# Optimization experiments

Measured on AMD Instinct MI355X. Metric: run time of the kernel, lower is better.

## Reference

```python
import jax, jax.numpy as jnp
import numpy as np

B = 2097152  # number of Gaussians


def setup_inputs() -> dict:
    key = jax.random.key(0)
    k1, k2, k3, k4, k5, k6 = jax.random.split(key, 6)
    return {
        "loc1": jax.random.normal(k1, (B, 3), dtype=jnp.float32),
        "scale1": jax.random.uniform(k2, (B, 3), dtype=jnp.float32),
        "rot_matrix1": jax.random.normal(k3, (B, 3, 3), dtype=jnp.float32),
        "loc2": jax.random.normal(k4, (B, 3), dtype=jnp.float32),
        "scale2": jax.random.uniform(k5, (B, 3), dtype=jnp.float32),
        "rot_matrix2": jax.random.normal(k6, (B, 3, 3), dtype=jnp.float32),
    }


def reference(loc1, scale1, rot_matrix1, loc2, scale2, rot_matrix2):
    # ||mu1 - mu2||^2  -> (B,)
    loc_diff2 = jnp.sum((loc1 - loc2) ** 2, axis=-1)

    # cov2 = R2 diag(scale2) R2^T  -> (B,3,3)
    cov2 = jnp.einsum("bij,bj,bkj->bik", rot_matrix2, scale2, rot_matrix2)
    # cov2 rotated into frame of Gaussian 1: R1^T cov2 R1  -> (B,3,3)
    cov2_R1 = jnp.einsum("bji,bjk,bkl->bil", rot_matrix1, cov2, rot_matrix1)

    # E = diag(sqrt(s1)) cov2_R1 diag(sqrt(s1)), then symmetrize
    s1_sqrt = jnp.sqrt(scale1)  # (B,3)
    E = s1_sqrt[:, :, None] * cov2_R1 * s1_sqrt[:, None, :]
    E = (E + jnp.swapaxes(E, 1, 2)) * 0.5

    # trace of matrix sqrt via eigenvalues: sum (lambda^2)^(1/4) = sum |lambda|^(1/2)
    E_eig = jnp.linalg.eigvalsh(E)  # (B,3)
    E_sqrt_trace = jnp.sum(jnp.sqrt(jnp.sqrt(E_eig ** 2)), axis=-1)

    cov_wasserstein = jnp.sum(scale1, axis=-1) + jnp.sum(scale2, axis=-1) - 2.0 * E_sqrt_trace
    cov_wasserstein = jnp.maximum(cov_wasserstein, 0.0)
    return jnp.sqrt(loc_diff2 + cov_wasserstein)
```

## Files before the change

kernel.cpp:

```cpp
#include <hip/hip_runtime.h>
#include <math.h>

#define BLK 256

__global__ __launch_bounds__(BLK, 8) void wasserstein_kernel(
    const float* __restrict__ loc1,   const float* __restrict__ scale1,
    const float* __restrict__ rot1,   const float* __restrict__ loc2,
    const float* __restrict__ scale2, const float* __restrict__ rot2,
    float* __restrict__ out)
{
    __shared__ float smem[BLK * 18];
    float* sR1 = smem;
    float* sR2 = smem + BLK * 9;

    const int tid = threadIdx.x;
    const long long blockStart = (long long)blockIdx.x * BLK;
    const long long idx = blockStart + tid;

    {
        const float4* g4;
        float4* l4;

        g4 = reinterpret_cast<const float4*>(rot1 + blockStart * 9);
        l4 = reinterpret_cast<float4*>(sR1);
#pragma unroll
        for (int i = 0; i < BLK * 9 / 4 / BLK + 1; ++i) {
            int j = tid + i * BLK;
            if (j < BLK * 9 / 4) l4[j] = g4[j];
        }

        g4 = reinterpret_cast<const float4*>(rot2 + blockStart * 9);
        l4 = reinterpret_cast<float4*>(sR2);
#pragma unroll
        for (int i = 0; i < BLK * 9 / 4 / BLK + 1; ++i) {
            int j = tid + i * BLK;
            if (j < BLK * 9 / 4) l4[j] = g4[j];
        }
    }

    const float l1x = loc1[idx * 3 + 0], l1y = loc1[idx * 3 + 1], l1z = loc1[idx * 3 + 2];
    const float l2x = loc2[idx * 3 + 0], l2y = loc2[idx * 3 + 1], l2z = loc2[idx * 3 + 2];
    const float s1a = scale1[idx * 3 + 0], s1b = scale1[idx * 3 + 1], s1c = scale1[idx * 3 + 2];
    const float s2a = scale2[idx * 3 + 0], s2b = scale2[idx * 3 + 1], s2c = scale2[idx * 3 + 2];

    __syncthreads();

    const float dx = l1x - l2x, dy = l1y - l2y, dz = l1z - l2z;
    const float loc_diff2 = dx * dx + dy * dy + dz * dz;

    float R1[9], R2[9];
#pragma unroll
    for (int k = 0; k < 9; ++k) R1[k] = sR1[tid * 9 + k];
#pragma unroll
    for (int k = 0; k < 9; ++k) R2[k] = sR2[tid * 9 + k];

    const float m00 = s2a * R2[0] * R2[0] + s2b * R2[1] * R2[1] + s2c * R2[2] * R2[2];
    const float m01 = s2a * R2[0] * R2[3] + s2b * R2[1] * R2[4] + s2c * R2[2] * R2[5];
    const float m02 = s2a * R2[0] * R2[6] + s2b * R2[1] * R2[7] + s2c * R2[2] * R2[8];
    const float m11 = s2a * R2[3] * R2[3] + s2b * R2[4] * R2[4] + s2c * R2[5] * R2[5];
    const float m12 = s2a * R2[3] * R2[6] + s2b * R2[4] * R2[7] + s2c * R2[5] * R2[8];
    const float m22 = s2a * R2[6] * R2[6] + s2b * R2[7] * R2[7] + s2c * R2[8] * R2[8];

    float A[9];
    A[0] = m00 * R1[0] + m01 * R1[3] + m02 * R1[6];
    A[1] = m00 * R1[1] + m01 * R1[4] + m02 * R1[7];
    A[2] = m00 * R1[2] + m01 * R1[5] + m02 * R1[8];
    A[3] = m01 * R1[0] + m11 * R1[3] + m12 * R1[6];
    A[4] = m01 * R1[1] + m11 * R1[4] + m12 * R1[7];
    A[5] = m01 * R1[2] + m11 * R1[5] + m12 * R1[8];
    A[6] = m02 * R1[0] + m12 * R1[3] + m22 * R1[6];
    A[7] = m02 * R1[1] + m12 * R1[4] + m22 * R1[7];
    A[8] = m02 * R1[2] + m12 * R1[5] + m22 * R1[8];

    float T[9];
    T[0] = R1[0] * A[0] + R1[3] * A[3] + R1[6] * A[6];
    T[1] = R1[0] * A[1] + R1[3] * A[4] + R1[6] * A[7];
    T[2] = R1[0] * A[2] + R1[3] * A[5] + R1[6] * A[8];
    T[3] = R1[1] * A[0] + R1[4] * A[3] + R1[7] * A[6];
    T[4] = R1[1] * A[1] + R1[4] * A[4] + R1[7] * A[7];
    T[5] = R1[1] * A[2] + R1[4] * A[5] + R1[7] * A[8];
    T[6] = R1[2] * A[0] + R1[5] * A[3] + R1[8] * A[6];
    T[7] = R1[2] * A[1] + R1[5] * A[4] + R1[8] * A[7];
    T[8] = R1[2] * A[2] + R1[5] * A[5] + R1[8] * A[8];

    const float sq0 = sqrtf(s1a), sq1 = sqrtf(s1b), sq2 = sqrtf(s1c);
    const float e00 = s1a * T[0];
    const float e11 = s1b * T[4];
    const float e22 = s1c * T[8];
    const float e01 = 0.5f * sq0 * sq1 * (T[1] + T[3]);
    const float e02 = 0.5f * sq0 * sq2 * (T[2] + T[6]);
    const float e12 = 0.5f * sq1 * sq2 * (T[5] + T[7]);

    const float q  = (e00 + e11 + e22) * (1.0f / 3.0f);
    const float p1 = e01 * e01 + e02 * e02 + e12 * e12;
    const float d0 = e00 - q, d1 = e11 - q, d2 = e22 - q;
    const float p2 = d0 * d0 + d1 * d1 + d2 * d2 + 2.0f * p1;

    float trace_sqrt;
    if (p2 > 1e-24f) {
        const float p   = sqrtf(p2 * (1.0f / 6.0f));
        const float inv = 1.0f / p;
        const float b00 = d0 * inv, b11 = d1 * inv, b22 = d2 * inv;
        const float b01 = e01 * inv, b02 = e02 * inv, b12 = e12 * inv;
        float detB = b00 * (b11 * b22 - b12 * b12)
                   - b01 * (b01 * b22 - b12 * b02)
                   + b02 * (b01 * b12 - b11 * b02);
        float r = 0.5f * detB;
        r = fminf(fmaxf(r, -1.0f), 1.0f);
        const float phi  = acosf(r) * (1.0f / 3.0f);
        const float twop = 2.0f * p;
        const float eig1 = q + twop * cosf(phi);
        const float eig3 = q + twop * cosf(phi + 2.0943951023931953f);
        const float eig2 = 3.0f * q - eig1 - eig3;
        trace_sqrt = sqrtf(fabsf(eig1)) + sqrtf(fabsf(eig2)) + sqrtf(fabsf(eig3));
    } else {
        trace_sqrt = 3.0f * sqrtf(fabsf(q));
    }

    float cov_w = (s1a + s1b + s1c) + (s2a + s2b + s2c) - 2.0f * trace_sqrt;
    cov_w = fmaxf(cov_w, 0.0f);
    out[idx] = sqrtf(loc_diff2 + cov_w);
}

extern "C" void kernel_launch(void* const* d_in, const int* in_sizes, int n_in,
                              void* d_out, int out_size, void* d_ws, size_t ws_size,
                              hipStream_t stream) {
    const float* loc1   = (const float*)d_in[0];
    const float* scale1 = (const float*)d_in[1];
    const float* rot1   = (const float*)d_in[2];
    const float* loc2   = (const float*)d_in[3];
    const float* scale2 = (const float*)d_in[4];
    const float* rot2   = (const float*)d_in[5];
    float* out = (float*)d_out;

    const int B = in_sizes[0] / 3;
    const int grid = B / BLK;

    wasserstein_kernel<<<grid, BLK, 0, stream>>>(loc1, scale1, rot1,
                                                 loc2, scale2, rot2, out);
}
```

Baseline: 240.2 us.

## Process four elements per thread with software-pipelined loads and characteristic-polynomial eigen solve

Result: no change. 241.6 us (+0.6%).

```diff
diff --git a/kernel.cpp b/kernel.cpp
--- a/kernel.cpp
+++ b/kernel.cpp
@@ -3,123 +3,121 @@
 
 #define BLK 256
 
-__global__ __launch_bounds__(BLK, 8) void wasserstein_kernel(
+struct Elem {
+    float l1[3], l2[3], s1[3], s2[3], R1[9], R2[9];
+};
+
+__device__ __forceinline__ void load_elem(
+    const float* __restrict__ loc1, const float* __restrict__ scale1,
+    const float* __restrict__ rot1, const float* __restrict__ loc2,
+    const float* __restrict__ scale2, const float* __restrict__ rot2,
+    int idx, Elem& e)
+{
+    __builtin_memcpy(e.R1, rot1   + (size_t)idx * 9, 36);
+    __builtin_memcpy(e.R2, rot2   + (size_t)idx * 9, 36);
+    __builtin_memcpy(e.l1, loc1   + (size_t)idx * 3, 12);
+    __builtin_memcpy(e.l2, loc2   + (size_t)idx * 3, 12);
+    __builtin_memcpy(e.s1, scale1 + (size_t)idx * 3, 12);
+    __builtin_memcpy(e.s2, scale2 + (size_t)idx * 3, 12);
+}
+
+__device__ __forceinline__ float compute(const Elem& e)
+{
+    const float dx = e.l1[0] - e.l2[0];
+    const float dy = e.l1[1] - e.l2[1];
+    const float dz = e.l1[2] - e.l2[2];
+    const float ld2 = dx * dx + dy * dy + dz * dz;
+
+    const float* R1 = e.R1;
+    const float* R2 = e.R2;
+    const float sa = e.s1[0], sb = e.s1[1], sc = e.s1[2];
+    const float ua = e.s2[0], ub = e.s2[1], uc = e.s2[2];
+
+    const float m00 = ua * R2[0] * R2[0] + ub * R2[1] * R2[1] + uc * R2[2] * R2[2];
+    const float m01 = ua * R2[0] * R2[3] + ub * R2[1] * R2[4] + uc * R2[2] * R2[5];
+    const float m02 = ua * R2[0] * R2[6] + ub * R2[1] * R2[7] + uc * R2[2] * R2[8];
+    const float m11 = ua * R2[3] * R2[3] + ub * R2[4] * R2[4] + uc * R2[5] * R2[5];
+    const float m12 = ua * R2[3] * R2[6] + ub * R2[4] * R2[7] + uc * R2[5] * R2[8];
+    const float m22 = ua * R2[6] * R2[6] + ub * R2[7] * R2[7] + uc * R2[8] * R2[8];
+
+    const float A0 = m00 * R1[0] + m01 * R1[3] + m02 * R1[6];
+    const float A1 = m00 * R1[1] + m01 * R1[4] + m02 * R1[7];
+    const float A2 = m00 * R1[2] + m01 * R1[5] + m02 * R1[8];
+    const float A3 = m01 * R1[0] + m11 * R1[3] + m12 * R1[6];
+    const float A4 = m01 * R1[1] + m11 * R1[4] + m12 * R1[7];
+    const float A5 = m01 * R1[2] + m11 * R1[5] + m12 * R1[8];
+    const float A6 = m02 * R1[0] + m12 * R1[3] + m22 * R1[6];
+    const float A7 = m02 * R1[1] + m12 * R1[4] + m22 * R1[7];
+    const float A8 = m02 * R1[2] + m12 * R1[5] + m22 * R1[8];
+
+    const float t00 = R1[0] * A0 + R1[3] * A3 + R1[6] * A6;
+    const float t01 = R1[0] * A1 + R1[3] * A4 + R1[6] * A7;
+    const float t02 = R1[0] * A2 + R1[3] * A5 + R1[6] * A8;
+    const float t11 = R1[1] * A1 + R1[4] * A4 + R1[7] * A7;
+    const float t12 = R1[1] * A2 + R1[4] * A5 + R1[7] * A8;
+    const float t22 = R1[2] * A2 + R1[5] * A5 + R1[8] * A8;
+
+    const float c2 = t00 * sa + t11 * sb + t22 * sc;
+    const float g2 = t00 * t00 * sa * sa + t11 * t11 * sb * sb + t22 * t22 * sc * sc
+                   + 2.0f * (t01 * t01 * sa * sb + t02 * t02 * sa * sc + t12 * t12 * sb * sc);
+    const float c1 = 0.5f * (c2 * c2 - g2);
+    const float detT = t00 * (t11 * t22 - t12 * t12)
+                     - t01 * (t01 * t22 - t12 * t02)
+                     + t02 * (t01 * t12 - t11 * t02);
+    const float c0 = detT * sa * sb * sc;
+
+    const float m  = c2 * (1.0f / 3.0f);
+    const float p  = c1 - c2 * m;
+    const float q  = c1 * m - 2.0f * m * m * m - c0;
+    const float s  = __builtin_amdgcn_sqrtf(fmaxf(-p * (1.0f / 3.0f), 0.0f));
+    const float s3 = 2.0f * s * s * s;
+    const float inv = __builtin_amdgcn_rcpf(fmaxf(s3, 1e-30f));
+    float u = -q * inv;
+    u = fminf(fmaxf(u, -1.0f), 1.0f);
+
+    const float au = fabsf(u);
+    const float rr = __builtin_amdgcn_sqrtf(1.0f - au) *
+        (1.5707288f + au * (-0.2121144f + au * (0.0742610f + au * (-0.0187293f))));
+    const float ac = (u < 0.0f) ? (3.14159265358979f - rr) : rr;
+
+    const float phi = ac * (1.0f / (3.0f * 6.283185307179586f));
+    const float x0 = 2.0f * s * __builtin_amdgcn_cosf(phi);
+    const float x1 = 2.0f * s * __builtin_amdgcn_cosf(phi - (1.0f / 3.0f));
+    const float e0 = x0 + m;
+    const float e1 = x1 + m;
+    const float e2 = c2 - e0 - e1;
+
+    const float tr = __builtin_amdgcn_sqrtf(fabsf(e0))
+                   + __builtin_amdgcn_sqrtf(fabsf(e1))
+                   + __builtin_amdgcn_sqrtf(fabsf(e2));
+
+    float cw = (sa + sb + sc) + (ua + ub + uc) - 2.0f * tr;
+    cw = fmaxf(cw, 0.0f);
+    return __builtin_amdgcn_sqrtf(ld2 + cw);
+}
+
+__global__ __launch_bounds__(BLK, 4) void wasserstein_kernel(
     const float* __restrict__ loc1,   const float* __restrict__ scale1,
     const float* __restrict__ rot1,   const float* __restrict__ loc2,
     const float* __restrict__ scale2, const float* __restrict__ rot2,
-    float* __restrict__ out)
+    float* __restrict__ out, int S)
 {
-    __shared__ float smem[BLK * 18];
-    float* sR1 = smem;
-    float* sR2 = smem + BLK * 9;
+    const int t = blockIdx.x * BLK + threadIdx.x;
 
-    const int tid = threadIdx.x;
-    const long long blockStart = (long long)blockIdx.x * BLK;
-    const long long idx = blockStart + tid;
+    Elem a, b;
+    load_elem(loc1, scale1, rot1, loc2, scale2, rot2, t, a);
+    load_elem(loc1, scale1, rot1, loc2, scale2, rot2, t + S, b);
 
-    {
-        const float4* g4;
-        float4* l4;
+    const float r0 = compute(a);
+    load_elem(loc1, scale1, rot1, loc2, scale2, rot2, t + 2 * S, a);
+    out[t] = r0;
 
-        g4 = reinterpret_cast<const float4*>(rot1 + blockStart * 9);
-        l4 = reinterpret_cast<float4*>(sR1);
-#pragma unroll
-        for (int i = 0; i < BLK * 9 / 4 / BLK + 1; ++i) {
-            int j = tid + i * BLK;
-            if (j < BLK * 9 / 4) l4[j] = g4[j];
-        }
+    const float r1 = compute(b);
+    load_elem(loc1, scale1, rot1, loc2, scale2, rot2, t + 3 * S, b);
+    out[t + S] = r1;
 
-        g4 = reinterpret_cast<const float4*>(rot2 + blockStart * 9);
-        l4 = reinterpret_cast<float4*>(sR2);
-#pragma unroll
-        for (int i = 0; i < BLK * 9 / 4 / BLK + 1; ++i) {
-            int j = tid + i * BLK;
-            if (j < BLK * 9 / 4) l4[j] = g4[j];
-        }
-    }
-
-    const float l1x = loc1[idx * 3 + 0], l1y = loc1[idx * 3 + 1], l1z = loc1[idx * 3 + 2];
-    const float l2x = loc2[idx * 3 + 0], l2y = loc2[idx * 3 + 1], l2z = loc2[idx * 3 + 2];
-    const float s1a = scale1[idx * 3 + 0], s1b = scale1[idx * 3 + 1], s1c = scale1[idx * 3 + 2];
-    const float s2a = scale2[idx * 3 + 0], s2b = scale2[idx * 3 + 1], s2c = scale2[idx * 3 + 2];
-
-    __syncthreads();
-
-    const float dx = l1x - l2x, dy = l1y - l2y, dz = l1z - l2z;
-    const float loc_diff2 = dx * dx + dy * dy + dz * dz;
-
-    float R1[9], R2[9];
-#pragma unroll
-    for (int k = 0; k < 9; ++k) R1[k] = sR1[tid * 9 + k];
-#pragma unroll
-    for (int k = 0; k < 9; ++k) R2[k] = sR2[tid * 9 + k];
-
-    const float m00 = s2a * R2[0] * R2[0] + s2b * R2[1] * R2[1] + s2c * R2[2] * R2[2];
-    const float m01 = s2a * R2[0] * R2[3] + s2b * R2[1] * R2[4] + s2c * R2[2] * R2[5];
-    const float m02 = s2a * R2[0] * R2[6] + s2b * R2[1] * R2[7] + s2c * R2[2] * R2[8];
-    const float m11 = s2a * R2[3] * R2[3] + s2b * R2[4] * R2[4] + s2c * R2[5] * R2[5];
-    const float m12 = s2a * R2[3] * R2[6] + s2b * R2[4] * R2[7] + s2c * R2[5] * R2[8];
-    const float m22 = s2a * R2[6] * R2[6] + s2b * R2[7] * R2[7] + s2c * R2[8] * R2[8];
-
-    float A[9];
-    A[0] = m00 * R1[0] + m01 * R1[3] + m02 * R1[6];
-    A[1] = m00 * R1[1] + m01 * R1[4] + m02 * R1[7];
-    A[2] = m00 * R1[2] + m01 * R1[5] + m02 * R1[8];
-    A[3] = m01 * R1[0] + m11 * R1[3] + m12 * R1[6];
-    A[4] = m01 * R1[1] + m11 * R1[4] + m12 * R1[7];
-    A[5] = m01 * R1[2] + m11 * R1[5] + m12 * R1[8];
-    A[6] = m02 * R1[0] + m12 * R1[3] + m22 * R1[6];
-    A[7] = m02 * R1[1] + m12 * R1[4] + m22 * R1[7];
-    A[8] = m02 * R1[2] + m12 * R1[5] + m22 * R1[8];
-
-    float T[9];
-    T[0] = R1[0] * A[0] + R1[3] * A[3] + R1[6] * A[6];
-    T[1] = R1[0] * A[1] + R1[3] * A[4] + R1[6] * A[7];
-    T[2] = R1[0] * A[2] + R1[3] * A[5] + R1[6] * A[8];
-    T[3] = R1[1] * A[0] + R1[4] * A[3] + R1[7] * A[6];
-    T[4] = R1[1] * A[1] + R1[4] * A[4] + R1[7] * A[7];
-    T[5] = R1[1] * A[2] + R1[4] * A[5] + R1[7] * A[8];
-    T[6] = R1[2] * A[0] + R1[5] * A[3] + R1[8] * A[6];
-    T[7] = R1[2] * A[1] + R1[5] * A[4] + R1[8] * A[7];
-    T[8] = R1[2] * A[2] + R1[5] * A[5] + R1[8] * A[8];
-
-    const float sq0 = sqrtf(s1a), sq1 = sqrtf(s1b), sq2 = sqrtf(s1c);
-    const float e00 = s1a * T[0];
-    const float e11 = s1b * T[4];
-    const float e22 = s1c * T[8];
-    const float e01 = 0.5f * sq0 * sq1 * (T[1] + T[3]);
-    const float e02 = 0.5f * sq0 * sq2 * (T[2] + T[6]);
-    const float e12 = 0.5f * sq1 * sq2 * (T[5] + T[7]);
-
-    const float q  = (e00 + e11 + e22) * (1.0f / 3.0f);
-    const float p1 = e01 * e01 + e02 * e02 + e12 * e12;
-    const float d0 = e00 - q, d1 = e11 - q, d2 = e22 - q;
-    const float p2 = d0 * d0 + d1 * d1 + d2 * d2 + 2.0f * p1;
-
-    float trace_sqrt;
-    if (p2 > 1e-24f) {
-        const float p   = sqrtf(p2 * (1.0f / 6.0f));
-        const float inv = 1.0f / p;
-        const float b00 = d0 * inv, b11 = d1 * inv, b22 = d2 * inv;
-        const float b01 = e01 * inv, b02 = e02 * inv, b12 = e12 * inv;
-        float detB = b00 * (b11 * b22 - b12 * b12)
-                   - b01 * (b01 * b22 - b12 * b02)
-                   + b02 * (b01 * b12 - b11 * b02);
-        float r = 0.5f * detB;
-        r = fminf(fmaxf(r, -1.0f), 1.0f);
-        const float phi  = acosf(r) * (1.0f / 3.0f);
-        const float twop = 2.0f * p;
-        const float eig1 = q + twop * cosf(phi);
-        const float eig3 = q + twop * cosf(phi + 2.0943951023931953f);
-        const float eig2 = 3.0f * q - eig1 - eig3;
-        trace_sqrt = sqrtf(fabsf(eig1)) + sqrtf(fabsf(eig2)) + sqrtf(fabsf(eig3));
-    } else {
-        trace_sqrt = 3.0f * sqrtf(fabsf(q));
-    }
-
-    float cov_w = (s1a + s1b + s1c) + (s2a + s2b + s2c) - 2.0f * trace_sqrt;
-    cov_w = fmaxf(cov_w, 0.0f);
-    out[idx] = sqrtf(loc_diff2 + cov_w);
+    out[t + 2 * S] = compute(a);
+    out[t + 3 * S] = compute(b);
 }
 
 extern "C" void kernel_launch(void* const* d_in, const int* in_sizes, int n_in,
@@ -134,8 +132,9 @@
     float* out = (float*)d_out;
 
     const int B = in_sizes[0] / 3;
-    const int grid = B / BLK;
+    const int S = B / 4;
+    const int grid = S / BLK;
 
     wasserstein_kernel<<<grid, BLK, 0, stream>>>(loc1, scale1, rot1,
-                                                 loc2, scale2, rot2, out);
+                                                 loc2, scale2, rot2, out, S);
 }
```
